# Optimization experiments

Hardware: AMD Instinct MI355X
Metric: run time of the kernel (lower is better)

The kernel has to match this reference:

```python
import jax, jax.numpy as jnp
import numpy as np

NUM_TOKENS = 1048576
TOP_K = 8
N_EXPERTS = 64
BLOCK = 128


def setup_inputs() -> dict:
    key = jax.random.key(0)
    topk_ids = jax.random.randint(key, (NUM_TOKENS, TOP_K), 0, N_EXPERTS, dtype=jnp.int32)
    return {"topk_ids": topk_ids, "num_experts": N_EXPERTS, "block_size": BLOCK}


def reference(topk_ids, num_experts, block_size):
    # Faithful re-implementation of sgl_kernel.moe_align_block_size with
    # E_eff = num_experts + 1 experts and pad_sorted_token_ids=True.
    flat = topk_ids.reshape(-1).astype(jnp.int32)
    T = flat.shape[0]                              # total routed tokens
    E = num_experts + 1                            # kernel is called with E+1
    M = T + E * (block_size - 1)                   # max_num_tokens_padded
    num_blocks = M // block_size                   # max_num_m_blocks

    # per-expert histogram and block-aligned (padded) counts
    counts = jnp.bincount(flat, length=E).astype(jnp.int32)
    padded = ((counts + block_size - 1) // block_size) * block_size

    cum_pad = jnp.cumsum(padded).astype(jnp.int32)          # inclusive padded cumsum
    off_pad = jnp.concatenate([jnp.zeros(1, jnp.int32), cum_pad[:-1]])  # exclusive
    cum_cnt = jnp.cumsum(counts).astype(jnp.int32)
    off_cnt = jnp.concatenate([jnp.zeros(1, jnp.int32), cum_cnt[:-1]])

    # stable sort token indices by expert id; rank within expert = sorted pos - start
    order = jnp.argsort(flat, stable=True).astype(jnp.int32)
    sorted_e = flat[order]
    j = jnp.arange(T, dtype=jnp.int32)
    pos = off_pad[sorted_e] + (j - off_cnt[sorted_e])

    # padding slots hold T (= topk_ids.numel()), matching pad_sorted_token_ids=True
    sorted_token_ids = jnp.full((M,), T, dtype=jnp.int32).at[pos].set(order)

    # expert id per M-block; blocks beyond the padded total stay 0 (torch.zeros init)
    bstart = jnp.arange(num_blocks, dtype=jnp.int32) * block_size
    eid = jnp.searchsorted(cum_pad, bstart, side='right').astype(jnp.int32)
    total = cum_pad[-1]
    expert_ids = jnp.where(bstart < total, eid, 0).astype(jnp.int32)

    num_tokens_post_pad = total.reshape(1).astype(jnp.int32)
    return sorted_token_ids, expert_ids, num_tokens_post_pad
```

## Files before the change

kernel.cpp:

```cpp
#include <hip/hip_runtime.h>
#include <stdint.h>

#define NE 64
#define E  65
#define BLK 128
#define WPB 4
#define THREADS 256
#define TPB 4096
#define CHB 64

__global__ void __launch_bounds__(THREADS, 8) k_hist(const int* __restrict__ topk,
                                                     int* __restrict__ bcnt) {
    __shared__ int hist[WPB][NE];
    const int tid = threadIdx.x, w = tid >> 6, lane = tid & 63;
    hist[w][lane] = 0;
    const int base = blockIdx.x * TPB + w * 1024;
#pragma unroll
    for (int it = 0; it < 4; ++it) {
        int4 v = *(const int4*)(topk + base + it * 256 + lane * 4);
        atomicAdd(&hist[w][v.x & 63], 1);
        atomicAdd(&hist[w][v.y & 63], 1);
        atomicAdd(&hist[w][v.z & 63], 1);
        atomicAdd(&hist[w][v.w & 63], 1);
    }
    __syncthreads();
    if (tid < NE)
        bcnt[blockIdx.x * NE + tid] =
            hist[0][tid] + hist[1][tid] + hist[2][tid] + hist[3][tid];
}

__global__ void k_scan1(int* __restrict__ bcnt, int* __restrict__ ctot) {
    __shared__ int tile[CHB * NE];
    const int c = blockIdx.x, tid = threadIdx.x;
    for (int i = tid; i < CHB * NE; i += THREADS) tile[i] = bcnt[c * CHB * NE + i];
    __syncthreads();
    if (tid < NE) {
        int acc = 0;
#pragma unroll 8
        for (int j = 0; j < CHB; ++j) { int o = tile[j * NE + tid]; tile[j * NE + tid] = acc; acc += o; }
        ctot[c * NE + tid] = acc;
    }
    __syncthreads();
    for (int i = tid; i < CHB * NE; i += THREADS) bcnt[c * CHB * NE + i] = tile[i];
}

__global__ void k_scan2(int* __restrict__ ctot, int* __restrict__ counts,
                        int* __restrict__ off_pad, int* __restrict__ cum_pad,
                        int* __restrict__ npp, int nc) {
    __shared__ int ct[32 * NE];
    const int tid = threadIdx.x;
    for (int i = tid; i < nc * NE; i += THREADS) ct[i] = ctot[i];
    __syncthreads();
    if (tid < NE) {
        int acc = 0;
        for (int c = 0; c < nc; ++c) { int o = ct[c * NE + tid]; ct[c * NE + tid] = acc; acc += o; }
        counts[tid] = acc;
    }
    if (tid == NE) counts[NE] = 0;
    __syncthreads();
    for (int i = tid; i < nc * NE; i += THREADS) ctot[i] = ct[i];
    if (tid == 0) {
        int run = 0;
        for (int e = 0; e < E; ++e) {
            int p = (counts[e] + BLK - 1) & ~(BLK - 1);
            off_pad[e] = run;
            run += p;
            cum_pad[e] = run;
        }
        *npp = run;
    }
}

__global__ void __launch_bounds__(THREADS) k_sort(
        const int* __restrict__ topk, const int* __restrict__ bpre,
        const int* __restrict__ ctot, const int* __restrict__ counts,
        const int* __restrict__ off_pad, const int* __restrict__ cum_pad,
        int* __restrict__ sorted, int* __restrict__ eids,
        int nb, int M, int T, int epb) {
    __shared__ int lrun[WPB][NE];
    __shared__ int wt[WPB][NE];
    __shared__ int sbuf[TPB];
    __shared__ int cps[E];
    const int tid = threadIdx.x, w = tid >> 6, lane = tid & 63;
    const int b = blockIdx.x, c = b / CHB;

    if (tid < E) cps[tid] = cum_pad[tid];
    lrun[w][lane] = 0;

    const int wstart = b * TPB + w * 1024;

    int packed[16];
#pragma unroll
    for (int it = 0; it < 16; ++it) {
        int e = topk[wstart + it * 64 + lane] & 63;
        int r = atomicAdd(&lrun[w][e], 1);
        packed[it] = (e << 10) | r;
    }
    wt[w][lane] = lrun[w][lane];
    __syncthreads();

    int woff = 0, btot = 0;
#pragma unroll
    for (int w2 = 0; w2 < WPB; ++w2) { int v = wt[w2][lane]; woff += (w2 < w) ? v : 0; btot += v; }
    int incl = btot;
#pragma unroll
    for (int d = 1; d < 64; d <<= 1) { int t = __shfl_up(incl, d); if (lane >= d) incl += t; }
    int loc = incl - btot;
    int dbase = off_pad[lane] + ctot[c * NE + lane] + bpre[b * NE + lane] - loc;
    int S = loc + woff;

    const int wloc = w * 1024;
#pragma unroll
    for (int it = 0; it < 16; ++it) {
        int e = packed[it] >> 10;
        int r = packed[it] & 1023;
        int pos = (__shfl(S, e) + r) & (TPB - 1);
        sbuf[pos] = (e << 12) | (wloc + it * 64 + lane);
    }
    __syncthreads();

    const int bstart = b * TPB;
#pragma unroll
    for (int k = 0; k < 16; ++k) {
        int j = k * THREADS + tid;
        int p = sbuf[j];
        int e = (p >> 12) & 63;
        int d = __shfl(dbase, e);
        sorted[d + j] = bstart + (p & 0xfff);
    }

    int total = cps[NE];
    if (tid < epb) {
        int j = b * epb + tid;
        if (j < nb) {
            int bs2 = j * BLK, r = 0;
            if (bs2 < total) {
                int lo = 0, hi = E;
                while (lo < hi) { int mid = (lo + hi) >> 1; if (cps[mid] <= bs2) lo = mid + 1; else hi = mid; }
                r = lo;
            }
            eids[j] = r;
        }
    }
    if (b < E) {
        int cc = counts[b];
        int pe = (cc + BLK - 1) & ~(BLK - 1);
        int len = pe - cc;
        if (tid < len) sorted[off_pad[b] + cc + tid] = T;
    } else if (b < E + 33) {
        int i = total + (b - E) * THREADS + tid;
        if (i < M) sorted[i] = T;
    }
}

extern "C" void kernel_launch(void* const* d_in, const int* in_sizes, int n_in,
                              void* d_out, int out_size, void* d_ws, size_t ws_size,
                              hipStream_t stream) {
    const int* topk = (const int*)d_in[0];
    const int T = in_sizes[0];
    const int M = T + E * (BLK - 1);
    const int nb = M / BLK;

    int* out = (int*)d_out;
    int* sorted = out;
    int* expert_ids = out + M;
    int* npp = out + M + nb;

    const int NB = T / TPB;
    const int NC = NB / CHB;
    const int epb = (nb + NB - 1) / NB;

    int* bcnt    = (int*)d_ws;
    int* ctot    = bcnt + (size_t)NB * NE;
    int* counts  = ctot + (size_t)NC * NE;
    int* off_pad = counts + E;
    int* cum_pad = off_pad + E;

    k_hist<<<NB, THREADS, 0, stream>>>(topk, bcnt);
    k_scan1<<<NC, THREADS, 0, stream>>>(bcnt, ctot);
    k_scan2<<<1, THREADS, 0, stream>>>(ctot, counts, off_pad, cum_pad, npp, NC);
    k_sort<<<NB, THREADS, 0, stream>>>(topk, bcnt, ctot, counts, off_pad, cum_pad,
                                       sorted, expert_ids, nb, M, T, epb);
}
```

Before: 38.55 us.

## Fuse histogram, scans and scatter into one cooperative kernel with grid syncs

```diff
diff --git a/kernel.cpp b/kernel.cpp
--- a/kernel.cpp
+++ b/kernel.cpp
@@ -1,13 +1,138 @@
 #include <hip/hip_runtime.h>
+#include <hip/hip_cooperative_groups.h>
 #include <stdint.h>
+
+namespace cg = cooperative_groups;
 
 #define NE 64
 #define E  65
 #define BLK 128
 #define WPB 4
 #define THREADS 256
+
+#define FTPB 8192
+#define FNB  1024
+#define FITS 32
+#define FCHB 64
+#define FNC  16
+
 #define TPB 4096
 #define CHB 64
+
+__global__ void __launch_bounds__(THREADS) k_fused(
+        const int* __restrict__ topk, int* __restrict__ bcnt, int* __restrict__ ctot,
+        int* __restrict__ sorted, int* __restrict__ eids, int* __restrict__ npp,
+        int nb, int M, int T, int epb) {
+    __shared__ int lrun[WPB][NE];
+    __shared__ int wt[WPB][NE];
+    __shared__ int sbuf[FTPB];
+    __shared__ int cps[E];
+    const int tid = threadIdx.x, w = tid >> 6, lane = tid & 63;
+    const int b = blockIdx.x, c = b >> 6;
+    cg::grid_group grid = cg::this_grid();
+
+    lrun[w][lane] = 0;
+    const int wstart = b * FTPB + w * 2048;
+
+    int packed[FITS];
+#pragma unroll
+    for (int it = 0; it < FITS; ++it) {
+        int e = topk[wstart + it * 64 + lane] & 63;
+        int r = atomicAdd(&lrun[w][e], 1);
+        packed[it] = (e << 11) | r;
+    }
+    wt[w][lane] = lrun[w][lane];
+    __syncthreads();
+
+    int woff = 0, btot = 0;
+#pragma unroll
+    for (int w2 = 0; w2 < WPB; ++w2) { int v = wt[w2][lane]; woff += (w2 < w) ? v : 0; btot += v; }
+    if (w == 0) bcnt[b * NE + lane] = btot;
+    int incl = btot;
+#pragma unroll
+    for (int d = 1; d < 64; d <<= 1) { int t = __shfl_up(incl, d); if (lane >= d) incl += t; }
+    int loc = incl - btot;
+    int S = loc + woff;
+
+    grid.sync();
+
+    if (b < FNC) {
+        for (int i = tid; i < FCHB * NE; i += THREADS) sbuf[i] = bcnt[b * FCHB * NE + i];
+        __syncthreads();
+        if (tid < NE) {
+            int acc = 0;
+#pragma unroll 8
+            for (int j = 0; j < FCHB; ++j) { int o = sbuf[j * NE + tid]; sbuf[j * NE + tid] = acc; acc += o; }
+            ctot[b * NE + tid] = acc;
+        }
+        __syncthreads();
+        for (int i = tid; i < FCHB * NE; i += THREADS) bcnt[b * FCHB * NE + i] = sbuf[i];
+    }
+
+    grid.sync();
+
+    int ct_pre = 0, cnt_tot = 0;
+#pragma unroll
+    for (int k = 0; k < FNC; ++k) {
+        int v = ctot[k * NE + lane];
+        ct_pre += (k < c) ? v : 0;
+        cnt_tot += v;
+    }
+    int padded = (cnt_tot + BLK - 1) & ~(BLK - 1);
+    int incl2 = padded;
+#pragma unroll
+    for (int d = 1; d < 64; d <<= 1) { int t = __shfl_up(incl2, d); if (lane >= d) incl2 += t; }
+    int off_lane = incl2 - padded;
+    int total = __shfl(incl2, 63);
+    if (w == 0) cps[lane] = incl2;
+    if (tid == 0) cps[NE] = total;
+
+    int dbase = off_lane + ct_pre + bcnt[b * NE + lane] - loc;
+
+    const int wloc = w * 2048;
+#pragma unroll
+    for (int it = 0; it < FITS; ++it) {
+        int e = packed[it] >> 11;
+        int r = packed[it] & 2047;
+        int pos = (__shfl(S, e) + r) & (FTPB - 1);
+        sbuf[pos] = (e << 13) | (wloc + it * 64 + lane);
+    }
+    __syncthreads();
+
+    const int bstart = b * FTPB;
+#pragma unroll
+    for (int k = 0; k < FITS; ++k) {
+        int j = k * THREADS + tid;
+        int p = sbuf[j];
+        int e = (p >> 13) & 63;
+        int d = __shfl(dbase, e);
+        sorted[d + j] = bstart + (p & (FTPB - 1));
+    }
+
+    if (tid < epb) {
+        int j = b * epb + tid;
+        if (j < nb) {
+            int bs2 = j * BLK, r = 0;
+            if (bs2 < total) {
+                int lo = 0, hi = E;
+                while (lo < hi) { int mid = (lo + hi) >> 1; if (cps[mid] <= bs2) lo = mid + 1; else hi = mid; }
+                r = lo;
+            }
+            eids[j] = r;
+        }
+    }
+    if (b < NE) {
+        int cc = __shfl(cnt_tot, b);
+        int ob = __shfl(off_lane, b);
+        int pe = (cc + BLK - 1) & ~(BLK - 1);
+        int len = pe - cc;
+        if (tid < len) sorted[ob + cc + tid] = T;
+    } else if (b >= E && b < E + 33) {
+        int i = total + (b - E) * THREADS + tid;
+        if (i < M) sorted[i] = T;
+    }
+    if (b == 0 && tid == 0) *npp = total;
+}
 
 __global__ void __launch_bounds__(THREADS, 8) k_hist(const int* __restrict__ topk,
                                                      int* __restrict__ bcnt) {
@@ -63,9 +188,7 @@
         int run = 0;
         for (int e = 0; e < E; ++e) {
             int p = (counts[e] + BLK - 1) & ~(BLK - 1);
-            off_pad[e] = run;
-            run += p;
-            cum_pad[e] = run;
+            off_pad[e] = run; run += p; cum_pad[e] = run;
         }
         *npp = run;
     }
@@ -83,12 +206,9 @@
     __shared__ int cps[E];
     const int tid = threadIdx.x, w = tid >> 6, lane = tid & 63;
     const int b = blockIdx.x, c = b / CHB;
-
     if (tid < E) cps[tid] = cum_pad[tid];
     lrun[w][lane] = 0;
-
     const int wstart = b * TPB + w * 1024;
-
     int packed[16];
 #pragma unroll
     for (int it = 0; it < 16; ++it) {
@@ -98,7 +218,6 @@
     }
     wt[w][lane] = lrun[w][lane];
     __syncthreads();
-
     int woff = 0, btot = 0;
 #pragma unroll
     for (int w2 = 0; w2 < WPB; ++w2) { int v = wt[w2][lane]; woff += (w2 < w) ? v : 0; btot += v; }
@@ -108,7 +227,6 @@
     int loc = incl - btot;
     int dbase = off_pad[lane] + ctot[c * NE + lane] + bpre[b * NE + lane] - loc;
     int S = loc + woff;
-
     const int wloc = w * 1024;
 #pragma unroll
     for (int it = 0; it < 16; ++it) {
@@ -118,7 +236,6 @@
         sbuf[pos] = (e << 12) | (wloc + it * 64 + lane);
     }
     __syncthreads();
-
     const int bstart = b * TPB;
 #pragma unroll
     for (int k = 0; k < 16; ++k) {
@@ -128,8 +245,7 @@
         int d = __shfl(dbase, e);
         sorted[d + j] = bstart + (p & 0xfff);
     }
-
-    int total = cps[NE];
+    int total = cps[NE - 1];
     if (tid < epb) {
         int j = b * epb + tid;
         if (j < nb) {
@@ -166,11 +282,41 @@
     int* expert_ids = out + M;
     int* npp = out + M + nb;
 
+    int* bcnt = (int*)d_ws;
+
+    bool fused_ok = (T == FNB * FTPB);
+    if (fused_ok) {
+        size_t need = ((size_t)FNB * NE + (size_t)FNC * NE) * sizeof(int);
+        if (need > ws_size) fused_ok = false;
+    }
+    if (fused_ok) {
+        int maxb = 0;
+        if (hipOccupancyMaxActiveBlocksPerMultiprocessor(&maxb, k_fused, THREADS, 0) != hipSuccess)
+            fused_ok = false;
+        int dev = 0, cus = 0;
+        hipGetDevice(&dev);
+        if (fused_ok && hipDeviceGetAttribute(&cus, hipDeviceAttributeMultiprocessorCount, dev) != hipSuccess)
+            fused_ok = false;
+        if (fused_ok && (long long)maxb * cus < FNB) fused_ok = false;
+    }
+
+    if (fused_ok) {
+        int* ctot = bcnt + (size_t)FNB * NE;
+        const int epb = (nb + FNB - 1) / FNB;
+        const int* topk_a = topk; int* bcnt_a = bcnt; int* ctot_a = ctot;
+        int* sorted_a = sorted; int* eids_a = expert_ids; int* npp_a = npp;
+        int nb_a = nb, M_a = M, T_a = T, epb_a = epb;
+        void* args[] = {(void*)&topk_a, (void*)&bcnt_a, (void*)&ctot_a,
+                        (void*)&sorted_a, (void*)&eids_a, (void*)&npp_a,
+                        (void*)&nb_a, (void*)&M_a, (void*)&T_a, (void*)&epb_a};
+        if (hipLaunchCooperativeKernel((void*)k_fused, dim3(FNB), dim3(THREADS),
+                                       args, 0, stream) == hipSuccess)
+            return;
+    }
+
     const int NB = T / TPB;
     const int NC = NB / CHB;
     const int epb = (nb + NB - 1) / NB;
-
-    int* bcnt    = (int*)d_ws;
     int* ctot    = bcnt + (size_t)NB * NE;
     int* counts  = ctot + (size_t)NC * NE;
     int* off_pad = counts + E;
```

After: 38.46 us. Within noise of the previous version (-0.2%).

## Fuse histogram, scans and scatter into one persistent kernel with flag-based prefix

Applied to the files above, without the earlier changes.

```diff
diff --git a/kernel.cpp b/kernel.cpp
--- a/kernel.cpp
+++ b/kernel.cpp
@@ -4,10 +4,163 @@
 #define NE 64
 #define E  65
 #define BLK 128
+
+#define THREADS1 512
+#define W1 8
+#define FITS 16
+#define TPB1 8192
+#define NB1 1024
+#define NG 16
+#define GSZ 64
+
+#define THREADS 256
 #define WPB 4
-#define THREADS 256
 #define TPB 4096
 #define CHB 64
+
+__device__ __forceinline__ int aload(const int* p) {
+    return __hip_atomic_load(p, __ATOMIC_RELAXED, __HIP_MEMORY_SCOPE_AGENT);
+}
+__device__ __forceinline__ void astore(int* p, int v) {
+    __hip_atomic_store(p, v, __ATOMIC_RELAXED, __HIP_MEMORY_SCOPE_AGENT);
+}
+
+__global__ void __launch_bounds__(THREADS1, 8) k_one(
+        const int* __restrict__ topk, int* __restrict__ flags, int* __restrict__ gflags,
+        int* __restrict__ agg, int* __restrict__ gagg,
+        int* __restrict__ sorted, int* __restrict__ eids, int* __restrict__ npp,
+        int nb, int M, int T, int epb) {
+    __shared__ int lrun[W1][NE];
+    __shared__ int wt[W1][NE];
+    __shared__ int sbuf[TPB1];
+    __shared__ int cps[E];
+    __shared__ int gpre_s[NE], cnts_s[NE];
+    const int tid = threadIdx.x, w = tid >> 6, lane = tid & 63;
+    const int b = blockIdx.x, g = b >> 6, j = b & 63;
+
+    lrun[w][lane] = 0;
+    const int wstart = b * TPB1 + w * 1024;
+
+    int packed[FITS];
+#pragma unroll
+    for (int it = 0; it < FITS; ++it) {
+        int e = topk[wstart + it * 64 + lane] & 63;
+        int r = atomicAdd(&lrun[w][e], 1);
+        packed[it] = (e << 10) | r;
+    }
+    wt[w][lane] = lrun[w][lane];
+    __syncthreads();
+
+    int btot = 0, woff = 0;
+#pragma unroll
+    for (int w2 = 0; w2 < W1; ++w2) { int v = wt[w2][lane]; btot += v; woff += (w2 < w) ? v : 0; }
+    int incl = btot;
+#pragma unroll
+    for (int d = 1; d < 64; d <<= 1) { int t = __shfl_up(incl, d); if (lane >= d) incl += t; }
+    int loc = incl - btot;
+    int S = loc + woff;
+
+    if (w == 0) {
+        astore(&agg[b * NE + lane], btot);
+        if (lane == 0)
+            __hip_atomic_store(&flags[b], 1, __ATOMIC_RELEASE, __HIP_MEMORY_SCOPE_AGENT);
+
+        if (j > 0) {
+            int ok;
+            do {
+                ok = 1;
+                if (lane < j &&
+                    __hip_atomic_load(&flags[g * GSZ + lane], __ATOMIC_ACQUIRE,
+                                      __HIP_MEMORY_SCOPE_AGENT) == 0) ok = 0;
+                if (__any(!ok)) __builtin_amdgcn_s_sleep(2);
+            } while (__any(!ok));
+        }
+        int gpre = 0;
+        for (int p = g * GSZ; p < b; ++p) gpre += aload(&agg[p * NE + lane]);
+
+        if (j == GSZ - 1) {
+            astore(&gagg[g * NE + lane], gpre + btot);
+            if (lane == 0)
+                __hip_atomic_store(&gflags[g], 1, __ATOMIC_RELEASE, __HIP_MEMORY_SCOPE_AGENT);
+        }
+        {
+            int ok;
+            do {
+                ok = 1;
+                if (lane < NG &&
+                    __hip_atomic_load(&gflags[lane], __ATOMIC_ACQUIRE,
+                                      __HIP_MEMORY_SCOPE_AGENT) == 0) ok = 0;
+                if (__any(!ok)) __builtin_amdgcn_s_sleep(2);
+            } while (__any(!ok));
+        }
+        int cnts = 0;
+#pragma unroll
+        for (int g2 = 0; g2 < NG; ++g2) {
+            int v = aload(&gagg[g2 * NE + lane]);
+            cnts += v;
+            gpre += (g2 < g) ? v : 0;
+        }
+        gpre_s[lane] = gpre;
+        cnts_s[lane] = cnts;
+    }
+    __syncthreads();
+
+    int gpre = gpre_s[lane], cnts = cnts_s[lane];
+    int padded = (cnts + BLK - 1) & ~(BLK - 1);
+    int incl2 = padded;
+#pragma unroll
+    for (int d = 1; d < 64; d <<= 1) { int t = __shfl_up(incl2, d); if (lane >= d) incl2 += t; }
+    int off_lane = incl2 - padded;
+    int total = __shfl(incl2, 63);
+    if (tid < NE) cps[tid] = incl2;
+    if (tid == 0) cps[NE] = total;
+
+    int dbase = off_lane + gpre - loc;
+
+    const int wloc = w * 1024;
+#pragma unroll
+    for (int it = 0; it < FITS; ++it) {
+        int e = packed[it] >> 10;
+        int r = packed[it] & 1023;
+        int pos = (__shfl(S, e) + r) & (TPB1 - 1);
+        sbuf[pos] = (e << 13) | (wloc + it * 64 + lane);
+    }
+    __syncthreads();
+
+    const int bstart = b * TPB1;
+#pragma unroll
+    for (int k = 0; k < TPB1 / THREADS1; ++k) {
+        int jj = k * THREADS1 + tid;
+        int p = sbuf[jj];
+        int e = (p >> 13) & 63;
+        int d = __shfl(dbase, e);
+        sorted[d + jj] = bstart + (p & (TPB1 - 1));
+    }
+
+    if (tid < epb) {
+        int jb = b * epb + tid;
+        if (jb < nb) {
+            int bs2 = jb * BLK, r = 0;
+            if (bs2 < total) {
+                int lo = 0, hi = E;
+                while (lo < hi) { int mid = (lo + hi) >> 1; if (cps[mid] <= bs2) lo = mid + 1; else hi = mid; }
+                r = lo;
+            }
+            eids[jb] = r;
+        }
+    }
+    if (b < NE) {
+        int cc = __shfl(cnts, b);
+        int ob = __shfl(off_lane, b);
+        int pe = (cc + BLK - 1) & ~(BLK - 1);
+        int len = pe - cc;
+        if (tid < len) sorted[ob + cc + tid] = T;
+    } else if (b >= E && b < E + 17) {
+        int i = total + (b - E) * THREADS1 + tid;
+        if (i < M) sorted[i] = T;
+    }
+    if (b == 0 && tid == 0) *npp = total;
+}
 
 __global__ void __launch_bounds__(THREADS, 8) k_hist(const int* __restrict__ topk,
                                                      int* __restrict__ bcnt) {
@@ -63,9 +216,7 @@
         int run = 0;
         for (int e = 0; e < E; ++e) {
             int p = (counts[e] + BLK - 1) & ~(BLK - 1);
-            off_pad[e] = run;
-            run += p;
-            cum_pad[e] = run;
+            off_pad[e] = run; run += p; cum_pad[e] = run;
         }
         *npp = run;
     }
@@ -83,12 +234,9 @@
     __shared__ int cps[E];
     const int tid = threadIdx.x, w = tid >> 6, lane = tid & 63;
     const int b = blockIdx.x, c = b / CHB;
-
     if (tid < E) cps[tid] = cum_pad[tid];
     lrun[w][lane] = 0;
-
     const int wstart = b * TPB + w * 1024;
-
     int packed[16];
 #pragma unroll
     for (int it = 0; it < 16; ++it) {
@@ -98,7 +246,6 @@
     }
     wt[w][lane] = lrun[w][lane];
     __syncthreads();
-
     int woff = 0, btot = 0;
 #pragma unroll
     for (int w2 = 0; w2 < WPB; ++w2) { int v = wt[w2][lane]; woff += (w2 < w) ? v : 0; btot += v; }
@@ -108,7 +255,6 @@
     int loc = incl - btot;
     int dbase = off_pad[lane] + ctot[c * NE + lane] + bpre[b * NE + lane] - loc;
     int S = loc + woff;
-
     const int wloc = w * 1024;
 #pragma unroll
     for (int it = 0; it < 16; ++it) {
@@ -118,7 +264,6 @@
         sbuf[pos] = (e << 12) | (wloc + it * 64 + lane);
     }
     __syncthreads();
-
     const int bstart = b * TPB;
 #pragma unroll
     for (int k = 0; k < 16; ++k) {
@@ -128,8 +273,7 @@
         int d = __shfl(dbase, e);
         sorted[d + j] = bstart + (p & 0xfff);
     }
-
-    int total = cps[NE];
+    int total = cps[NE - 1];
     if (tid < epb) {
         int j = b * epb + tid;
         if (j < nb) {
@@ -166,10 +310,34 @@
     int* expert_ids = out + M;
     int* npp = out + M + nb;
 
+    bool one_ok = (T == NB1 * TPB1);
+    size_t need1 = ((size_t)NB1 + NG + (size_t)NB1 * NE + (size_t)NG * NE) * sizeof(int);
+    if (need1 > ws_size) one_ok = false;
+    if (one_ok) {
+        int maxb = 0, cus = 0, dev = 0;
+        if (hipOccupancyMaxActiveBlocksPerMultiprocessor(&maxb, k_one, THREADS1, 0) != hipSuccess)
+            one_ok = false;
+        hipGetDevice(&dev);
+        if (one_ok && hipDeviceGetAttribute(&cus, hipDeviceAttributeMultiprocessorCount, dev) != hipSuccess)
+            one_ok = false;
+        if (one_ok && (long long)maxb * cus < NB1) one_ok = false;
+    }
+
+    if (one_ok) {
+        int* flags  = (int*)d_ws;
+        int* gflags = flags + NB1;
+        int* agg    = gflags + NG;
+        int* gagg   = agg + (size_t)NB1 * NE;
+        const int epb = (nb + NB1 - 1) / NB1;
+        hipMemsetAsync(flags, 0, (size_t)(NB1 + NG) * sizeof(int), stream);
+        k_one<<<NB1, THREADS1, 0, stream>>>(topk, flags, gflags, agg, gagg,
+                                            sorted, expert_ids, npp, nb, M, T, epb);
+        return;
+    }
+
     const int NB = T / TPB;
     const int NC = NB / CHB;
     const int epb = (nb + NB - 1) / NB;
-
     int* bcnt    = (int*)d_ws;
     int* ctot    = bcnt + (size_t)NB * NE;
     int* counts  = ctot + (size_t)NC * NE;
```

Measured after the change: 38.65 us. No clear change (+0.3%).

## Add fast path storing packed per-token ranks between rank and scatter kernels

Applied to the files above, without the earlier changes.

```diff
diff --git a/kernel.cpp b/kernel.cpp
--- a/kernel.cpp
+++ b/kernel.cpp
@@ -4,10 +4,166 @@
 #define NE 64
 #define E  65
 #define BLK 128
+#define CHB 64
+
+#define T1 512
+#define W1 8
+#define TPB1 8192
+#define NB1 1024
+#define NC1 16
+
+#define THREADS 256
 #define WPB 4
-#define THREADS 256
 #define TPB 4096
-#define CHB 64
+
+
+__global__ void __launch_bounds__(T1) k_rank(const int* __restrict__ topk,
+                                             uint32_t* __restrict__ packed,
+                                             int* __restrict__ wcnt,
+                                             int* __restrict__ bcnt) {
+    __shared__ int lrun[W1][NE];
+    const int tid = threadIdx.x, w = tid >> 6, lane = tid & 63;
+    const int b = blockIdx.x;
+    lrun[w][lane] = 0;
+    const int wstart = b * TPB1 + w * 1024;
+    uint32_t pk[8];
+#pragma unroll
+    for (int it = 0; it < 16; ++it) {
+        int e = topk[wstart + it * 64 + lane] & 63;
+        int r = atomicAdd(&lrun[w][e], 1);
+        uint32_t p = ((uint32_t)e << 10) | (uint32_t)r;
+        if (it & 1) pk[it >> 1] |= p; else pk[it >> 1] = p << 16;
+    }
+#pragma unroll
+    for (int q = 0; q < 8; ++q)
+        packed[(size_t)b * 4096 + w * 512 + q * 64 + lane] = pk[q];
+    wcnt[b * (W1 * NE) + w * NE + lane] = lrun[w][lane];
+    __syncthreads();
+    if (tid < NE) {
+        int s = 0;
+#pragma unroll
+        for (int w2 = 0; w2 < W1; ++w2) s += lrun[w2][tid];
+        bcnt[b * NE + tid] = s;
+    }
+}
+
+__global__ void k_scan1(int* __restrict__ bcnt, int* __restrict__ ctot) {
+    __shared__ int tile[CHB * NE];
+    const int c = blockIdx.x, tid = threadIdx.x;
+    for (int i = tid; i < CHB * NE; i += THREADS) tile[i] = bcnt[c * CHB * NE + i];
+    __syncthreads();
+    if (tid < NE) {
+        int acc = 0;
+#pragma unroll 8
+        for (int j = 0; j < CHB; ++j) { int o = tile[j * NE + tid]; tile[j * NE + tid] = acc; acc += o; }
+        ctot[c * NE + tid] = acc;
+    }
+    __syncthreads();
+    for (int i = tid; i < CHB * NE; i += THREADS) bcnt[c * CHB * NE + i] = tile[i];
+}
+
+__global__ void k_scan2(int* __restrict__ ctot, int* __restrict__ counts,
+                        int* __restrict__ off_pad, int* __restrict__ cum_pad,
+                        int* __restrict__ npp, int nc) {
+    __shared__ int ct[32 * NE];
+    const int tid = threadIdx.x;
+    for (int i = tid; i < nc * NE; i += THREADS) ct[i] = ctot[i];
+    __syncthreads();
+    if (tid < NE) {
+        int acc = 0;
+        for (int c = 0; c < nc; ++c) { int o = ct[c * NE + tid]; ct[c * NE + tid] = acc; acc += o; }
+        counts[tid] = acc;
+    }
+    if (tid == NE) counts[NE] = 0;
+    __syncthreads();
+    for (int i = tid; i < nc * NE; i += THREADS) ctot[i] = ct[i];
+    if (tid == 0) {
+        int run = 0;
+        for (int e = 0; e < E; ++e) {
+            int p = (counts[e] + BLK - 1) & ~(BLK - 1);
+            off_pad[e] = run; run += p; cum_pad[e] = run;
+        }
+        *npp = run;
+    }
+}
+
+__global__ void __launch_bounds__(T1) k_sort2(
+        const uint32_t* __restrict__ packed, const int* __restrict__ wcnt,
+        const int* __restrict__ bpre,
+        const int* __restrict__ ctot, const int* __restrict__ counts,
+        const int* __restrict__ off_pad, const int* __restrict__ cum_pad,
+        int* __restrict__ sorted, int* __restrict__ eids,
+        int nb, int M, int T, int epb) {
+    __shared__ int sbuf[TPB1];
+    __shared__ int cps[E];
+    const int tid = threadIdx.x, w = tid >> 6, lane = tid & 63;
+    const int b = blockIdx.x, c = b >> 6;
+    if (tid < E) cps[tid] = cum_pad[tid];
+
+    uint32_t pk[8];
+#pragma unroll
+    for (int q = 0; q < 8; ++q)
+        pk[q] = packed[(size_t)b * 4096 + w * 512 + q * 64 + lane];
+
+    int btot = 0, woff = 0;
+#pragma unroll
+    for (int w2 = 0; w2 < W1; ++w2) {
+        int v = wcnt[b * (W1 * NE) + w2 * NE + lane];
+        btot += v; woff += (w2 < w) ? v : 0;
+    }
+    int incl = btot;
+#pragma unroll
+    for (int d = 1; d < 64; d <<= 1) { int t = __shfl_up(incl, d); if (lane >= d) incl += t; }
+    int loc = incl - btot;
+    int S = loc + woff;
+    int dbase = off_pad[lane] + ctot[c * NE + lane] + bpre[b * NE + lane] - loc;
+
+    const int wloc = w * 1024;
+#pragma unroll
+    for (int q = 0; q < 8; ++q) {
+        uint32_t pw = pk[q];
+        int e0 = (int)(pw >> 26) & 63, r0 = (int)((pw >> 16) & 1023);
+        int e1 = (int)((pw >> 10) & 63), r1 = (int)(pw & 1023);
+        int p0 = (__shfl(S, e0) + r0) & (TPB1 - 1);
+        int p1 = (__shfl(S, e1) + r1) & (TPB1 - 1);
+        sbuf[p0] = (e0 << 13) | (wloc + (2 * q) * 64 + lane);
+        sbuf[p1] = (e1 << 13) | (wloc + (2 * q + 1) * 64 + lane);
+    }
+    __syncthreads();
+
+    const int bstart = b * TPB1;
+#pragma unroll
+    for (int k = 0; k < TPB1 / T1; ++k) {
+        int j = k * T1 + tid;
+        int p = sbuf[j];
+        int e = (p >> 13) & 63;
+        int d = __shfl(dbase, e);
+        sorted[d + j] = bstart + (p & (TPB1 - 1));
+    }
+
+    int total = cps[NE];
+    if (tid < epb) {
+        int jb = b * epb + tid;
+        if (jb < nb) {
+            int bs2 = jb * BLK, r = 0;
+            if (bs2 < total) {
+                int lo = 0, hi = E;
+                while (lo < hi) { int mid = (lo + hi) >> 1; if (cps[mid] <= bs2) lo = mid + 1; else hi = mid; }
+                r = lo;
+            }
+            eids[jb] = r;
+        }
+    }
+    if (b < NE) {
+        int cc = counts[b];
+        int pe = (cc + BLK - 1) & ~(BLK - 1);
+        int len = pe - cc;
+        if (tid < len) sorted[off_pad[b] + cc + tid] = T;
+    } else if (b >= E && b < E + 17) {
+        int i = total + (b - E) * T1 + tid;
+        if (i < M) sorted[i] = T;
+    }
+}
 
 __global__ void __launch_bounds__(THREADS, 8) k_hist(const int* __restrict__ topk,
                                                      int* __restrict__ bcnt) {
@@ -27,48 +183,6 @@
     if (tid < NE)
         bcnt[blockIdx.x * NE + tid] =
             hist[0][tid] + hist[1][tid] + hist[2][tid] + hist[3][tid];
-}
-
-__global__ void k_scan1(int* __restrict__ bcnt, int* __restrict__ ctot) {
-    __shared__ int tile[CHB * NE];
-    const int c = blockIdx.x, tid = threadIdx.x;
-    for (int i = tid; i < CHB * NE; i += THREADS) tile[i] = bcnt[c * CHB * NE + i];
-    __syncthreads();
-    if (tid < NE) {
-        int acc = 0;
-#pragma unroll 8
-        for (int j = 0; j < CHB; ++j) { int o = tile[j * NE + tid]; tile[j * NE + tid] = acc; acc += o; }
-        ctot[c * NE + tid] = acc;
-    }
-    __syncthreads();
-    for (int i = tid; i < CHB * NE; i += THREADS) bcnt[c * CHB * NE + i] = tile[i];
-}
-
-__global__ void k_scan2(int* __restrict__ ctot, int* __restrict__ counts,
-                        int* __restrict__ off_pad, int* __restrict__ cum_pad,
-                        int* __restrict__ npp, int nc) {
-    __shared__ int ct[32 * NE];
-    const int tid = threadIdx.x;
-    for (int i = tid; i < nc * NE; i += THREADS) ct[i] = ctot[i];
-    __syncthreads();
-    if (tid < NE) {
-        int acc = 0;
-        for (int c = 0; c < nc; ++c) { int o = ct[c * NE + tid]; ct[c * NE + tid] = acc; acc += o; }
-        counts[tid] = acc;
-    }
-    if (tid == NE) counts[NE] = 0;
-    __syncthreads();
-    for (int i = tid; i < nc * NE; i += THREADS) ctot[i] = ct[i];
-    if (tid == 0) {
-        int run = 0;
-        for (int e = 0; e < E; ++e) {
-            int p = (counts[e] + BLK - 1) & ~(BLK - 1);
-            off_pad[e] = run;
-            run += p;
-            cum_pad[e] = run;
-        }
-        *npp = run;
-    }
 }
 
 __global__ void __launch_bounds__(THREADS) k_sort(
@@ -83,12 +197,9 @@
     __shared__ int cps[E];
     const int tid = threadIdx.x, w = tid >> 6, lane = tid & 63;
     const int b = blockIdx.x, c = b / CHB;
-
     if (tid < E) cps[tid] = cum_pad[tid];
     lrun[w][lane] = 0;
-
     const int wstart = b * TPB + w * 1024;
-
     int packed[16];
 #pragma unroll
     for (int it = 0; it < 16; ++it) {
@@ -98,7 +209,6 @@
     }
     wt[w][lane] = lrun[w][lane];
     __syncthreads();
-
     int woff = 0, btot = 0;
 #pragma unroll
     for (int w2 = 0; w2 < WPB; ++w2) { int v = wt[w2][lane]; woff += (w2 < w) ? v : 0; btot += v; }
@@ -108,7 +218,6 @@
     int loc = incl - btot;
     int dbase = off_pad[lane] + ctot[c * NE + lane] + bpre[b * NE + lane] - loc;
     int S = loc + woff;
-
     const int wloc = w * 1024;
 #pragma unroll
     for (int it = 0; it < 16; ++it) {
@@ -118,7 +227,6 @@
         sbuf[pos] = (e << 12) | (wloc + it * 64 + lane);
     }
     __syncthreads();
-
     const int bstart = b * TPB;
 #pragma unroll
     for (int k = 0; k < 16; ++k) {
@@ -128,8 +236,7 @@
         int d = __shfl(dbase, e);
         sorted[d + j] = bstart + (p & 0xfff);
     }
-
-    int total = cps[NE];
+    int total = cps[NE - 1];
     if (tid < epb) {
         int j = b * epb + tid;
         if (j < nb) {
@@ -166,10 +273,33 @@
     int* expert_ids = out + M;
     int* npp = out + M + nb;
 
+    bool fast = (T == NB1 * TPB1);
+    size_t need = ((size_t)(T / 2) + (size_t)NB1 * W1 * NE + (size_t)NB1 * NE
+                   + (size_t)NC1 * NE + 3 * E) * sizeof(int);
+    if (need > ws_size) fast = false;
+
+    if (fast) {
+        uint32_t* packed = (uint32_t*)d_ws;
+        int* wcnt    = (int*)(packed + (size_t)T / 2);
+        int* bcnt    = wcnt + (size_t)NB1 * W1 * NE;
+        int* ctot    = bcnt + (size_t)NB1 * NE;
+        int* counts  = ctot + (size_t)NC1 * NE;
+        int* off_pad = counts + E;
+        int* cum_pad = off_pad + E;
+        const int epb = (nb + NB1 - 1) / NB1;
+
+        k_rank<<<NB1, T1, 0, stream>>>(topk, packed, wcnt, bcnt);
+        k_scan1<<<NC1, THREADS, 0, stream>>>(bcnt, ctot);
+        k_scan2<<<1, THREADS, 0, stream>>>(ctot, counts, off_pad, cum_pad, npp, NC1);
+        k_sort2<<<NB1, T1, 0, stream>>>(packed, wcnt, bcnt, ctot, counts,
+                                        off_pad, cum_pad, sorted, expert_ids,
+                                        nb, M, T, epb);
+        return;
+    }
+
     const int NB = T / TPB;
     const int NC = NB / CHB;
     const int epb = (nb + NB - 1) / NB;
-
     int* bcnt    = (int*)d_ws;
     int* ctot    = bcnt + (size_t)NB * NE;
     int* counts  = ctot + (size_t)NC * NE;
```

New measurement: 34.47 us. 10.6% less time.
